# Performance work log

Measured on AMD Instinct MI355X. Metric: run time of the kernel, lower is better.

The kernel has to match this reference:

```python
import jax, jax.numpy as jnp
import numpy as np

N_STEPS = 100  # t = linspace(1, 100, 100) -> dt = 1.0
DT = 1.0
NEG_SLOPE = 0.01  # torch LeakyReLU default


def setup_inputs() -> dict:
    key = jax.random.key(0)
    ks = jax.random.split(key, 6)
    B = 131072
    return {
        "x": jax.random.normal(ks[0], (B, 1), dtype=jnp.float32),
        "u": jax.random.normal(ks[1], (B, 1), dtype=jnp.float32),
        "W1": jax.random.normal(ks[2], (2, 4), dtype=jnp.float32) * 0.5,
        "b1": jax.random.normal(ks[3], (4,), dtype=jnp.float32) * 0.1,
        "W2": jax.random.normal(ks[4], (4, 1), dtype=jnp.float32) * 0.5,
        "b2": jax.random.normal(ks[5], (1,), dtype=jnp.float32) * 0.1,
    }


def reference(x, u, W1, b1, W2, b2):
    def dyn(s):  # s: [B,1] -> dx/dt: [B,1]
        z = jnp.concatenate((s, u), axis=-1)          # [B,2]
        h = z @ W1 + b1                               # [B,4]
        h = jnp.where(h >= 0, h, NEG_SLOPE * h)        # LeakyReLU
        return h @ W2 + b2                             # [B,1]

    def step(s, _):
        k1 = dyn(s)
        k2 = dyn(s + 0.5 * DT * k1)
        k3 = dyn(s + 0.5 * DT * k2)
        k4 = dyn(s + DT * k3)
        s_new = s + (DT / 6.0) * (k1 + 2.0 * k2 + 2.0 * k3 + k4)
        return s_new, s_new

    _, traj = jax.lax.scan(step, x, None, length=N_STEPS - 1)  # [99,B,1]
    pred = jnp.concatenate((x[None], traj), axis=0)            # [100,B,1]
    return jnp.transpose(pred, (1, 0, 2))                      # [B,100,1]
```

## Files before the change

### kernel.cpp

```cpp
#include <hip/hip_runtime.h>


#define NSTEP 100

__global__ __launch_bounds__(256, 2) void rk4_net_kernel(
    const float* __restrict__ x, const float* __restrict__ u,
    const float* __restrict__ W1, const float* __restrict__ b1,
    const float* __restrict__ W2, const float* __restrict__ b2,
    float* __restrict__ out, int B)
{
    const int b = blockIdx.x * blockDim.x + threadIdx.x;
    if (b >= B) return;

    const float A0 = W1[0], A1 = W1[1], A2 = W1[2], A3 = W1[3];
    const float U0 = W1[4], U1 = W1[5], U2 = W1[6], U3 = W1[7];
    const float w0 = W2[0], w1 = W2[1], w2 = W2[2], w3 = W2[3];
    const float bias2 = b2[0];

    const float uu = u[b];
    float s = x[b];

    const float C0 = fmaf(uu, U0, b1[0]);
    const float C1 = fmaf(uu, U1, b1[1]);
    const float C2 = fmaf(uu, U2, b1[2]);
    const float C3 = fmaf(uu, U3, b1[3]);

    const float al = 0.505f, be = 0.495f;
    const float wa0 = al * w0, wa1 = al * w1, wa2 = al * w2, wa3 = al * w3;
    const float wb0 = be * w0, wb1 = be * w1, wb2 = be * w2, wb3 = be * w3;

    auto dyn = [&](float sv) -> float {
        float h0 = fmaf(sv, A0, C0);
        float h1 = fmaf(sv, A1, C1);
        float h2 = fmaf(sv, A2, C2);
        float h3 = fmaf(sv, A3, C3);
        float p = fmaf(h0, wa0, bias2);
        float q = __builtin_fabsf(h0) * wb0;
        p = fmaf(h1, wa1, p);
        q = fmaf(__builtin_fabsf(h1), wb1, q);
        p = fmaf(h2, wa2, p);
        q = fmaf(__builtin_fabsf(h2), wb2, q);
        p = fmaf(h3, wa3, p);
        q = fmaf(__builtin_fabsf(h3), wb3, q);
        return p + q;
    };

    auto step = [&](float sv) -> float {
        float k1 = dyn(sv);
        float k2 = dyn(fmaf(0.5f, k1, sv));
        float k3 = dyn(fmaf(0.5f, k2, sv));
        float k4 = dyn(sv + k3);
        float sum = fmaf(2.0f, k2, k1);
        sum = fmaf(2.0f, k3, sum);
        sum += k4;
        return fmaf(0.16666667f, sum, sv);
    };

    float4* o4 = (float4*)(out + (size_t)b * NSTEP);

    float4 v;
    v.x = s;
    s = step(s); v.y = s;
    s = step(s); v.z = s;
    s = step(s); v.w = s;
    o4[0] = v;

#pragma unroll 1
    for (int c = 1; c < 25; ++c) {
        s = step(s); v.x = s;
        s = step(s); v.y = s;
        s = step(s); v.z = s;
        s = step(s); v.w = s;
        o4[c] = v;
    }
}

extern "C" void kernel_launch(void* const* d_in, const int* in_sizes, int n_in,
                              void* d_out, int out_size, void* d_ws, size_t ws_size,
                              hipStream_t stream) {
    const float* x  = (const float*)d_in[0];
    const float* u  = (const float*)d_in[1];
    const float* W1 = (const float*)d_in[2];
    const float* b1 = (const float*)d_in[3];
    const float* W2 = (const float*)d_in[4];
    const float* b2 = (const float*)d_in[5];
    float* out = (float*)d_out;

    const int B = in_sizes[0];
    const int block = 256;
    const int grid = (B + block - 1) / block;
    hipLaunchKernelGGL(rk4_net_kernel, dim3(grid), dim3(block), 0, stream,
                       x, u, W1, b1, W2, b2, out, B);
}
```

Before: 99.09 us.

## Fold linear leaky-ReLU term into scalar affine and process two elements per thread

Rewrites leaky-ReLU as a linear part plus an abs part, collapsing the linear contribution into a single s*P+Q per evaluation to cut FMAs. Each thread now integrates two batch elements with interleaved independent RK4 chains to expose instruction-level parallelism. This halves the thread count, which lowers occupancy and makes each thread's output stores less contiguous; odd batch sizes would drop the last element.

```diff
diff --git a/kernel.cpp b/kernel.cpp
--- a/kernel.cpp
+++ b/kernel.cpp
@@ -2,76 +2,97 @@
 
 
 #define NSTEP 100
+#define BLK 256
 
-__global__ __launch_bounds__(256, 2) void rk4_net_kernel(
+__global__ __launch_bounds__(BLK) void rk4_net_kernel(
     const float* __restrict__ x, const float* __restrict__ u,
     const float* __restrict__ W1, const float* __restrict__ b1,
     const float* __restrict__ W2, const float* __restrict__ b2,
     float* __restrict__ out, int B)
 {
-    const int b = blockIdx.x * blockDim.x + threadIdx.x;
-    if (b >= B) return;
+    const int i = blockIdx.x * BLK + threadIdx.x;
+    if (i >= (B >> 1)) return;
 
     const float A0 = W1[0], A1 = W1[1], A2 = W1[2], A3 = W1[3];
     const float U0 = W1[4], U1 = W1[5], U2 = W1[6], U3 = W1[7];
     const float w0 = W2[0], w1 = W2[1], w2 = W2[2], w3 = W2[3];
     const float bias2 = b2[0];
-
-    const float uu = u[b];
-    float s = x[b];
-
-    const float C0 = fmaf(uu, U0, b1[0]);
-    const float C1 = fmaf(uu, U1, b1[1]);
-    const float C2 = fmaf(uu, U2, b1[2]);
-    const float C3 = fmaf(uu, U3, b1[3]);
+    const float B0 = b1[0], B1 = b1[1], B2 = b1[2], B3 = b1[3];
 
     const float al = 0.505f, be = 0.495f;
     const float wa0 = al * w0, wa1 = al * w1, wa2 = al * w2, wa3 = al * w3;
     const float wb0 = be * w0, wb1 = be * w1, wb2 = be * w2, wb3 = be * w3;
+    float P = wa0 * A0;
+    P = fmaf(wa1, A1, P);
+    P = fmaf(wa2, A2, P);
+    P = fmaf(wa3, A3, P);
 
-    auto dyn = [&](float sv) -> float {
-        float h0 = fmaf(sv, A0, C0);
-        float h1 = fmaf(sv, A1, C1);
-        float h2 = fmaf(sv, A2, C2);
-        float h3 = fmaf(sv, A3, C3);
-        float p = fmaf(h0, wa0, bias2);
-        float q = __builtin_fabsf(h0) * wb0;
-        p = fmaf(h1, wa1, p);
-        q = fmaf(__builtin_fabsf(h1), wb1, q);
-        p = fmaf(h2, wa2, p);
-        q = fmaf(__builtin_fabsf(h2), wb2, q);
-        p = fmaf(h3, wa3, p);
-        q = fmaf(__builtin_fabsf(h3), wb3, q);
-        return p + q;
+    const float2 xx = ((const float2*)x)[i];
+    const float2 uu = ((const float2*)u)[i];
+
+    const float C00 = fmaf(uu.x, U0, B0), C01 = fmaf(uu.x, U1, B1),
+                C02 = fmaf(uu.x, U2, B2), C03 = fmaf(uu.x, U3, B3);
+    const float C10 = fmaf(uu.y, U0, B0), C11 = fmaf(uu.y, U1, B1),
+                C12 = fmaf(uu.y, U2, B2), C13 = fmaf(uu.y, U3, B3);
+    float Q0 = fmaf(wa0, C00, bias2);
+    Q0 = fmaf(wa1, C01, Q0); Q0 = fmaf(wa2, C02, Q0); Q0 = fmaf(wa3, C03, Q0);
+    float Q1 = fmaf(wa0, C10, bias2);
+    Q1 = fmaf(wa1, C11, Q1); Q1 = fmaf(wa2, C12, Q1); Q1 = fmaf(wa3, C13, Q1);
+
+    auto dyn = [&](float s, float c0, float c1, float c2, float c3,
+                   float Q) -> float {
+        float h0 = fmaf(s, A0, c0);
+        float h1 = fmaf(s, A1, c1);
+        float h2 = fmaf(s, A2, c2);
+        float h3 = fmaf(s, A3, c3);
+        float t0 = __builtin_fabsf(h0) * wb0;
+        float t1 = __builtin_fabsf(h1) * wb1;
+        t0 = fmaf(__builtin_fabsf(h2), wb2, t0);
+        t1 = fmaf(__builtin_fabsf(h3), wb3, t1);
+        float lin = fmaf(s, P, Q);
+        return lin + (t0 + t1);
     };
 
-    auto step = [&](float sv) -> float {
-        float k1 = dyn(sv);
-        float k2 = dyn(fmaf(0.5f, k1, sv));
-        float k3 = dyn(fmaf(0.5f, k2, sv));
-        float k4 = dyn(sv + k3);
+    auto step = [&](float s, float c0, float c1, float c2, float c3,
+                    float Q) -> float {
+        float k1 = dyn(s, c0, c1, c2, c3, Q);
+        float k2 = dyn(fmaf(0.5f, k1, s), c0, c1, c2, c3, Q);
+        float k3 = dyn(fmaf(0.5f, k2, s), c0, c1, c2, c3, Q);
+        float k4 = dyn(s + k3, c0, c1, c2, c3, Q);
         float sum = fmaf(2.0f, k2, k1);
         sum = fmaf(2.0f, k3, sum);
         sum += k4;
-        return fmaf(0.16666667f, sum, sv);
+        return fmaf(0.16666667f, sum, s);
     };
 
-    float4* o4 = (float4*)(out + (size_t)b * NSTEP);
+    float s0 = xx.x, s1 = xx.y;
 
-    float4 v;
-    v.x = s;
-    s = step(s); v.y = s;
-    s = step(s); v.z = s;
-    s = step(s); v.w = s;
-    o4[0] = v;
+    float4* o0 = (float4*)(out + (size_t)(2 * i) * NSTEP);
+    float4* o1 = (float4*)(out + (size_t)(2 * i + 1) * NSTEP);
+
+    float4 v0, v1;
+    v0.x = s0; v1.x = s1;
+    s0 = step(s0, C00, C01, C02, C03, Q0); v0.y = s0;
+    s1 = step(s1, C10, C11, C12, C13, Q1); v1.y = s1;
+    s0 = step(s0, C00, C01, C02, C03, Q0); v0.z = s0;
+    s1 = step(s1, C10, C11, C12, C13, Q1); v1.z = s1;
+    s0 = step(s0, C00, C01, C02, C03, Q0); v0.w = s0;
+    s1 = step(s1, C10, C11, C12, C13, Q1); v1.w = s1;
+    o0[0] = v0;
+    o1[0] = v1;
 
 #pragma unroll 1
     for (int c = 1; c < 25; ++c) {
-        s = step(s); v.x = s;
-        s = step(s); v.y = s;
-        s = step(s); v.z = s;
-        s = step(s); v.w = s;
-        o4[c] = v;
+        s0 = step(s0, C00, C01, C02, C03, Q0); v0.x = s0;
+        s1 = step(s1, C10, C11, C12, C13, Q1); v1.x = s1;
+        s0 = step(s0, C00, C01, C02, C03, Q0); v0.y = s0;
+        s1 = step(s1, C10, C11, C12, C13, Q1); v1.y = s1;
+        s0 = step(s0, C00, C01, C02, C03, Q0); v0.z = s0;
+        s1 = step(s1, C10, C11, C12, C13, Q1); v1.z = s1;
+        s0 = step(s0, C00, C01, C02, C03, Q0); v0.w = s0;
+        s1 = step(s1, C10, C11, C12, C13, Q1); v1.w = s1;
+        o0[c] = v0;
+        o1[c] = v1;
     }
 }
 
@@ -87,8 +108,8 @@
     float* out = (float*)d_out;
 
     const int B = in_sizes[0];
-    const int block = 256;
-    const int grid = (B + block - 1) / block;
-    hipLaunchKernelGGL(rk4_net_kernel, dim3(grid), dim3(block), 0, stream,
+    const int pairs = B >> 1;
+    const int grid = (pairs + BLK - 1) / BLK;
+    hipLaunchKernelGGL(rk4_net_kernel, dim3(grid), dim3(BLK), 0, stream,
                        x, u, W1, b1, W2, b2, out, B);
 }
```

New measurement: 103.5 us. +4.5%, slower.
